# Performance work log

Measured on AMD Instinct MI355X. Metric: run time of the kernel, lower is better.

Reference implementation:

```python
import jax, jax.numpy as jnp
import numpy as np

B, N, E, H = 2, 2048, 1024, 16
D = E // H


def setup_inputs() -> dict:
    key = jax.random.key(0)
    ks = jax.random.split(key, 10)
    s = 0.02  # small init so softmax is well-conditioned
    return {
        "x": jax.random.normal(ks[0], (B, N, E), jnp.float32),
        "y": jax.random.normal(ks[1], (B, N, E), jnp.float32),
        # W stored as [in, out]; torch Linear computes x @ W_t.T + b, equivalent here.
        "Wq": jax.random.normal(ks[2], (E, E), jnp.float32) * s,
        "bq": jax.random.normal(ks[3], (E,), jnp.float32) * s,
        "Wk": jax.random.normal(ks[4], (E, E), jnp.float32) * s,
        "bk": jax.random.normal(ks[5], (E,), jnp.float32) * s,
        "Wv": jax.random.normal(ks[6], (E, E), jnp.float32) * s,
        "bv": jax.random.normal(ks[7], (E,), jnp.float32) * s,
        "Wo": jax.random.normal(ks[8], (E, E), jnp.float32) * s,
        "bo": jax.random.normal(ks[9], (E,), jnp.float32) * s,
    }


def _split_heads(t):
    # [b, n, (h d)] -> [b, h, n, d]
    b, n, e = t.shape
    return t.reshape(b, n, H, D).transpose(0, 2, 1, 3)


def reference(x, y, Wq, bq, Wk, bk, Wv, bv, Wo, bo):
    q = _split_heads(x @ Wq + bq)          # [b,h,n,d]
    k = _split_heads(y @ Wk + bk)
    v = _split_heads(y @ Wv + bv)
    energy = jnp.einsum('bhqd,bhkd->bhqk', q, k)            # [b,h,n,n]
    # Faithful quirk: softmax first, then divide by sqrt(emb_size).
    scaling = jnp.asarray(E, x.dtype) ** 0.5
    att = jax.nn.softmax(energy, axis=-1) / scaling
    out = jnp.einsum('bhqk,bhkd->bhqd', att, v)             # [b,h,n,d]
    out = out.transpose(0, 2, 1, 3).reshape(x.shape[0], x.shape[1], E)
    return out @ Wo + bo
```

## Files before the change

kernel.cpp:

```cpp
#include <hip/hip_runtime.h>
#include <stdint.h>

#define BATCH 2
#define SEQ   2048
#define EMB   1024
#define NH    16
#define HD    64
#define MROWS (BATCH*SEQ)
#define LOG2E 1.4426950408889634f

using bf16x8 = __attribute__((ext_vector_type(8))) short;
using f32x4  = __attribute__((ext_vector_type(4))) float;
using f32x16 = __attribute__((ext_vector_type(16))) float;

__device__ __forceinline__ unsigned short f2bf(float f) {
  __bf16 b = (__bf16)f;
  return __builtin_bit_cast(unsigned short, b);
}

__device__ __forceinline__ unsigned int cvtpk_bf16(float lo, float hi) {
  unsigned int w;
  asm("v_cvt_pk_bf16_f32 %0, %1, %2" : "=v"(w) : "v"(lo), "v"(hi));
  return w;
}

#if __has_builtin(__builtin_amdgcn_exp2f)
__device__ __forceinline__ float fast_exp2(float x) { return __builtin_amdgcn_exp2f(x); }
#else
__device__ __forceinline__ float fast_exp2(float x) {
  float r;
  asm("v_exp_f32 %0, %1\n\ts_nop 1" : "=v"(r) : "v"(x));
  return r;
}
#endif

__device__ __forceinline__ void async_load16(const void* g, void* l) {
  __builtin_amdgcn_global_load_lds(
      (__attribute__((address_space(1))) void*)g,
      (__attribute__((address_space(3))) void*)l,
      16, 0, 0);
}

__global__ __launch_bounds__(256) void convert_kernel(
    const float* __restrict__ in, unsigned short* __restrict__ out, int n4) {
  int i = blockIdx.x * blockDim.x + threadIdx.x;
  if (i >= n4) return;
  const float4 v = reinterpret_cast<const float4*>(in)[i];
  ushort4 o;
  o.x = f2bf(v.x); o.y = f2bf(v.y); o.z = f2bf(v.z); o.w = f2bf(v.w);
  reinterpret_cast<ushort4*>(out)[i] = o;
}

__global__ __launch_bounds__(256) void transw_kernel(
    const float* __restrict__ Wq, const float* __restrict__ Wk,
    const float* __restrict__ Wv, const float* __restrict__ Wo,
    unsigned short* __restrict__ WtAll) {
  const int z = blockIdx.z;
  const float* W = (z == 0) ? Wq : (z == 1) ? Wk : (z == 2) ? Wv : Wo;
  unsigned short* Wt = WtAll + (size_t)z * EMB * EMB;
  __shared__ unsigned short tile[64][65];
  const int tc = threadIdx.x & 15;
  const int tr = threadIdx.x >> 4;
  const int n0 = blockIdx.x * 64, k0 = blockIdx.y * 64;
#pragma unroll
  for (int rr = 0; rr < 4; ++rr) {
    const int row = rr * 16 + tr;
    float4 v = *reinterpret_cast<const float4*>(W + (size_t)(k0 + row) * EMB + n0 + tc * 4);
    tile[tc * 4 + 0][row] = f2bf(v.x);
    tile[tc * 4 + 1][row] = f2bf(v.y);
    tile[tc * 4 + 2][row] = f2bf(v.z);
    tile[tc * 4 + 3][row] = f2bf(v.w);
  }
  __syncthreads();
#pragma unroll
  for (int rr = 0; rr < 4; ++rr) {
    const int row = rr * 16 + tr;
    ushort4 o;
    o.x = tile[row][tc * 4 + 0];
    o.y = tile[row][tc * 4 + 1];
    o.z = tile[row][tc * 4 + 2];
    o.w = tile[row][tc * 4 + 3];
    *reinterpret_cast<ushort4*>(Wt + (size_t)(n0 + row) * EMB + k0 + tc * 4) = o;
  }
}

#define BM 128
#define BN 128
#define BK 32

__global__ __launch_bounds__(256, 2) void gemm_kernel(
    const unsigned short* __restrict__ xb,
    const unsigned short* __restrict__ yb,
    const unsigned short* __restrict__ attnb,
    const unsigned short* __restrict__ WtAll,
    const float* __restrict__ bq, const float* __restrict__ bk,
    const float* __restrict__ bv, const float* __restrict__ bo,
    unsigned short* __restrict__ Qb, unsigned short* __restrict__ Kb,
    unsigned short* __restrict__ Vt, float* __restrict__ dout,
    int phase) {
  __shared__ __align__(16) unsigned short As[BM * BK];
  __shared__ __align__(16) unsigned short Bs[BN * BK];

  const int z = blockIdx.z;
  const unsigned short* A;
  const unsigned short* Bt;
  const float* bias;
  int mode;
  if (phase == 0) {
    A    = (z == 0) ? xb : yb;
    Bt   = WtAll + (size_t)z * EMB * EMB;
    bias = (z == 0) ? bq : (z == 1) ? bk : bv;
    mode = z;
  } else {
    A = attnb; Bt = WtAll + (size_t)3 * EMB * EMB; bias = bo; mode = 3;
  }

  const int tid = threadIdx.x;
  const int lane = tid & 63, wid = tid >> 6;
  const int wr = wid >> 1, wc = wid & 1;
  const int l15 = lane & 15, l4 = lane >> 4;
  const int m0 = blockIdx.y * BM, n0 = blockIdx.x * BN;

  const int crow = tid >> 2;
  const int cslot = tid & 3;

  f32x4 acc[4][4] = {};

  for (int kt = 0; kt < EMB; kt += BK) {
#pragma unroll
    for (int it = 0; it < 2; ++it)
      async_load16(A + (size_t)(m0 + it * 64 + crow) * EMB + kt + cslot * 8,
                   (char*)As + it * 4096 + wid * 1024);
#pragma unroll
    for (int it = 0; it < 2; ++it)
      async_load16(Bt + (size_t)(n0 + it * 64 + crow) * EMB + kt + cslot * 8,
                   (char*)Bs + it * 4096 + wid * 1024);
    __syncthreads();

    bf16x8 af[4], bfr[4];
#pragma unroll
    for (int i = 0; i < 4; ++i) {
      af[i]  = *reinterpret_cast<const bf16x8*>((const char*)As + (wr * 64 + i * 16 + l15) * 64 + l4 * 16);
      bfr[i] = *reinterpret_cast<const bf16x8*>((const char*)Bs + (wc * 64 + i * 16 + l15) * 64 + l4 * 16);
    }
#pragma unroll
    for (int i = 0; i < 4; ++i)
#pragma unroll
      for (int j = 0; j < 4; ++j)
        acc[i][j] = __builtin_amdgcn_mfma_f32_16x16x32_bf16(af[i], bfr[j], acc[i][j], 0, 0, 0);
    __syncthreads();
  }

#pragma unroll
  for (int i = 0; i < 4; ++i) {
#pragma unroll
    for (int j = 0; j < 4; ++j) {
      const int col = n0 + wc * 64 + j * 16 + l15;
      const float bsv = bias[col];
#pragma unroll
      for (int r = 0; r < 4; ++r) {
        const int row = m0 + wr * 64 + i * 16 + l4 * 4 + r;
        const float v = acc[i][j][r] + bsv;
        if (mode == 3) {
          dout[(size_t)row * EMB + col] = v;
        } else {
          const int b = row >> 11, n = row & (SEQ - 1);
          const int h = col >> 6, d = col & (HD - 1);
          if (mode == 0)
            Qb[(((size_t)(b * NH + h)) * SEQ + n) * HD + d] = f2bf(v);
          else if (mode == 1)
            Kb[(((size_t)(b * NH + h)) * SEQ + n) * HD + d] = f2bf(v * LOG2E);
          else
            Vt[(((size_t)(b * NH + h)) * HD + d) * SEQ + n] = f2bf(v);
        }
      }
    }
  }
}

#define KVB 64
#define NT  (SEQ/KVB)

__global__ __launch_bounds__(256, 2) void flash_kernel(
    const unsigned short* __restrict__ Qb,
    const unsigned short* __restrict__ Kb,
    const unsigned short* __restrict__ Vt,
    unsigned short* __restrict__ attnb) {
  __shared__ __align__(16) char Ks[2][8192];
  __shared__ __align__(16) char Vs[2][8192];

  const int tid = threadIdx.x;
  const int lane = tid & 63, wid = tid >> 6;
  const int l31 = lane & 31, hi = lane >> 5;

  const int lin = blockIdx.x;
  const int swz = (lin & 7) * 64 + (lin >> 3);
  const int bh = swz >> 4;
  const int qt = swz & 15;
  const int bb = bh >> 4, hh = bh & 15;
  const int q0 = qt * 128 + wid * 32;

  const unsigned short* Qp = Qb + (size_t)bh * SEQ * HD;
  const unsigned short* Kp = Kb + (size_t)bh * SEQ * HD;
  const unsigned short* Vp = Vt + (size_t)bh * HD * SEQ;

  const int srow = tid >> 3;
  const int sslot = tid & 7;

  bf16x8 qf[4];
#pragma unroll
  for (int kt = 0; kt < 4; ++kt)
    qf[kt] = *reinterpret_cast<const bf16x8*>(Qp + (size_t)(q0 + l31) * HD + kt * 16 + hi * 8);

#define STAGE(b, kv)                                                        \
  {                                                                         \
    _Pragma("unroll")                                                       \
    for (int it = 0; it < 2; ++it) {                                        \
      const int r = it * 32 + srow;                                         \
      async_load16(Kp + (size_t)((kv) + r) * HD + ((sslot ^ (r & 7)) * 8),  \
                   Ks[b] + it * 4096 + tid * 16);                           \
      async_load16(Vp + (size_t)r * SEQ + (kv) + ((sslot ^ (r & 7)) * 8),   \
                   Vs[b] + it * 4096 + tid * 16);                           \
    }                                                                       \
  }

  STAGE(0, 0)
  STAGE(1, KVB)

  f32x16 accO[2] = {};
  float mI = -1e30f, lI = 0.f;

  for (int t = 0; t < NT; ++t) {
    const int buf = t & 1;
    if (t < NT - 1) {
      asm volatile("s_waitcnt vmcnt(4)" ::: "memory");
    } else {
      asm volatile("s_waitcnt vmcnt(0)" ::: "memory");
    }
    __builtin_amdgcn_s_barrier();
    __builtin_amdgcn_sched_barrier(0);

    bf16x8 kf[2][4];
#pragma unroll
    for (int t2 = 0; t2 < 2; ++t2)
#pragma unroll
      for (int kt = 0; kt < 4; ++kt) {
        const int key = t2 * 32 + l31;
        kf[t2][kt] = *reinterpret_cast<const bf16x8*>(
            Ks[buf] + key * 128 + (((kt * 2 + hi) ^ (key & 7)) * 16));
      }
    f32x16 sc[2] = {};
#pragma unroll
    for (int t2 = 0; t2 < 2; ++t2)
#pragma unroll
      for (int kt = 0; kt < 4; ++kt)
        sc[t2] = __builtin_amdgcn_mfma_f32_32x32x16_bf16(kf[t2][kt], qf[kt], sc[t2], 0, 0, 0);

    float mown = sc[0][0];
#pragma unroll
    for (int t2 = 0; t2 < 2; ++t2)
#pragma unroll
      for (int r = 0; r < 16; ++r) mown = fmaxf(mown, sc[t2][r]);
    mown = fmaxf(mown, __shfl_xor(mown, 32));

    if (!__all(mown - mI <= 8.0f)) {
      const float mnew = fmaxf(mI, mown);
      const float scl = fast_exp2(mI - mnew);
      mI = mnew;
      lI *= scl;
#pragma unroll
      for (int dt = 0; dt < 2; ++dt)
#pragma unroll
        for (int r = 0; r < 16; ++r) accO[dt][r] *= scl;
    }

    float p[2][16];
    float ls = 0.f;
#pragma unroll
    for (int t2 = 0; t2 < 2; ++t2)
#pragma unroll
      for (int r = 0; r < 16; ++r) {
        p[t2][r] = fast_exp2(sc[t2][r] - mI);
        ls += p[t2][r];
      }
    ls += __shfl_xor(ls, 32);
    lI += ls;

    bf16x8 pf[4];
#pragma unroll
    for (int kt = 0; kt < 4; ++kt) {
      const int t2 = kt >> 1, g = (kt & 1) * 8;
      const unsigned int Aw = cvtpk_bf16(p[t2][g + 0], p[t2][g + 1]);
      const unsigned int Cw = cvtpk_bf16(p[t2][g + 2], p[t2][g + 3]);
      const unsigned int Bw = cvtpk_bf16(p[t2][g + 4], p[t2][g + 5]);
      const unsigned int Dw = cvtpk_bf16(p[t2][g + 6], p[t2][g + 7]);
      const unsigned int s1 = hi ? Aw : Bw;
      const unsigned int r1 = __shfl_xor(s1, 32);
      const unsigned int s2 = hi ? Cw : Dw;
      const unsigned int r2 = __shfl_xor(s2, 32);
      union { unsigned int u[4]; bf16x8 v; } cvt;
      cvt.u[0] = hi ? r1 : Aw;
      cvt.u[1] = hi ? r2 : Cw;
      cvt.u[2] = hi ? Bw : r1;
      cvt.u[3] = hi ? Dw : r2;
      pf[kt] = cvt.v;
    }

    bf16x8 vf[2][4];
#pragma unroll
    for (int dt = 0; dt < 2; ++dt)
#pragma unroll
      for (int kt = 0; kt < 4; ++kt) {
        const int d = dt * 32 + l31;
        vf[dt][kt] = *reinterpret_cast<const bf16x8*>(
            Vs[buf] + d * 128 + (((kt * 2 + hi) ^ (d & 7)) * 16));
      }
#pragma unroll
    for (int dt = 0; dt < 2; ++dt)
#pragma unroll
      for (int kt = 0; kt < 4; ++kt)
        accO[dt] = __builtin_amdgcn_mfma_f32_32x32x16_bf16(vf[dt][kt], pf[kt], accO[dt], 0, 0, 0);

    __builtin_amdgcn_sched_barrier(0);
    __builtin_amdgcn_s_barrier();
    __builtin_amdgcn_sched_barrier(0);

    if (t + 2 < NT) {
      STAGE(buf, (t + 2) * KVB)
    }
  }

  const float inv = 1.0f / (lI * 32.0f);
  const size_t obase = ((size_t)(bb * SEQ + q0 + l31)) * EMB + hh * HD;
#pragma unroll
  for (int dt = 0; dt < 2; ++dt)
#pragma unroll
    for (int rr = 0; rr < 4; ++rr) {
      ushort4 o;
      o.x = f2bf(accO[dt][rr * 4 + 0] * inv);
      o.y = f2bf(accO[dt][rr * 4 + 1] * inv);
      o.z = f2bf(accO[dt][rr * 4 + 2] * inv);
      o.w = f2bf(accO[dt][rr * 4 + 3] * inv);
      *reinterpret_cast<ushort4*>(attnb + obase + dt * 32 + 8 * rr + 4 * hi) = o;
    }
}

extern "C" void kernel_launch(void* const* d_in, const int* in_sizes, int n_in,
                              void* d_out, int out_size, void* d_ws, size_t ws_size,
                              hipStream_t stream) {
  (void)in_sizes; (void)n_in; (void)out_size;
  const float* x  = (const float*)d_in[0];
  const float* y  = (const float*)d_in[1];
  const float* Wq = (const float*)d_in[2];
  const float* bq = (const float*)d_in[3];
  const float* Wk = (const float*)d_in[4];
  const float* bk = (const float*)d_in[5];
  const float* Wv = (const float*)d_in[6];
  const float* bv = (const float*)d_in[7];
  const float* Wo = (const float*)d_in[8];
  const float* bo = (const float*)d_in[9];
  float* out = (float*)d_out;

  char* ws = (char*)d_ws;
  unsigned short* xb    = (unsigned short*)(ws + (size_t)(0u  << 20));
  unsigned short* yb    = (unsigned short*)(ws + (size_t)(8u  << 20));
  unsigned short* WtAll = (unsigned short*)(ws + (size_t)(16u << 20));
  unsigned short* Qb    = (unsigned short*)(ws + (size_t)(24u << 20));
  unsigned short* Kb    = (unsigned short*)(ws + (size_t)(32u << 20));
  unsigned short* Vt    = (unsigned short*)(ws + (size_t)(40u << 20));
  unsigned short* attnb = (unsigned short*)(ws + (size_t)(48u << 20));
  if (ws_size < ((size_t)56u << 20)) return;

  const int n4 = (BATCH * SEQ * EMB) / 4;
  hipLaunchKernelGGL(convert_kernel, dim3(n4 / 256), dim3(256), 0, stream, x, xb, n4);
  hipLaunchKernelGGL(convert_kernel, dim3(n4 / 256), dim3(256), 0, stream, y, yb, n4);
  hipLaunchKernelGGL(transw_kernel, dim3(16, 16, 4), dim3(256), 0, stream, Wq, Wk, Wv, Wo, WtAll);
  hipLaunchKernelGGL(gemm_kernel, dim3(EMB / BN, MROWS / BM, 3), dim3(256), 0, stream,
                     xb, yb, attnb, WtAll, bq, bk, bv, bo, Qb, Kb, Vt, out, 0);
  hipLaunchKernelGGL(flash_kernel, dim3(SEQ / 128 * BATCH * NH), dim3(256), 0, stream,
                     Qb, Kb, Vt, attnb);
  hipLaunchKernelGGL(gemm_kernel, dim3(EMB / BN, MROWS / BM, 1), dim3(256), 0, stream,
                     xb, yb, attnb, WtAll, bq, bk, bv, bo, Qb, Kb, Vt, out, 1);
}
```

Baseline: 145.6 us.

## Triple-buffer GEMM and flash-attention LDS stages; use permlane32 swap for cross-half exchange

Both the projection GEMM and the flash-attention loop now use a three-slot LDS ring. The load for step s+2 is issued right after the single barrier at the top of each iteration, so the second barrier per iteration goes away and global-to-LDS copies overlap compute. The flash kernel also replaces ds_bpermute-based __shfl_xor(…,32) exchanges for the max, the sum and the P fragment repacking with the permlane32_swap builtin when it is available. The cost is 50% more LDS per block, which may reduce occupancy, and the GEMM now waits with vmcnt counting.

```diff
diff --git a/kernel.cpp b/kernel.cpp
--- a/kernel.cpp
+++ b/kernel.cpp
@@ -33,6 +33,32 @@
   return r;
 }
 #endif
+
+__device__ __forceinline__ void swap32(unsigned int& a, unsigned int& b, int hi) {
+#if __has_builtin(__builtin_amdgcn_permlane32_swap)
+  (void)hi;
+  typedef unsigned int u32x2_t __attribute__((ext_vector_type(2)));
+  u32x2_t r = __builtin_amdgcn_permlane32_swap(a, b, false, false);
+  a = r[0]; b = r[1];
+#else
+  const unsigned int ca = __shfl_xor(a, 32), cb = __shfl_xor(b, 32);
+  const unsigned int na = hi ? cb : a;
+  const unsigned int nb = hi ? b : ca;
+  a = na; b = nb;
+#endif
+}
+
+__device__ __forceinline__ float xmax32(float x, int hi) {
+  unsigned int a = __builtin_bit_cast(unsigned int, x), b = a;
+  swap32(a, b, hi);
+  return fmaxf(__builtin_bit_cast(float, a), __builtin_bit_cast(float, b));
+}
+
+__device__ __forceinline__ float xadd32(float x, int hi) {
+  unsigned int a = __builtin_bit_cast(unsigned int, x), b = a;
+  swap32(a, b, hi);
+  return __builtin_bit_cast(float, a) + __builtin_bit_cast(float, b);
+}
 
 __device__ __forceinline__ void async_load16(const void* g, void* l) {
   __builtin_amdgcn_global_load_lds(
@@ -87,6 +113,7 @@
 #define BM 128
 #define BN 128
 #define BK 32
+#define NKS (EMB/BK)
 
 __global__ __launch_bounds__(256, 2) void gemm_kernel(
     const unsigned short* __restrict__ xb,
@@ -98,8 +125,8 @@
     unsigned short* __restrict__ Qb, unsigned short* __restrict__ Kb,
     unsigned short* __restrict__ Vt, float* __restrict__ dout,
     int phase) {
-  __shared__ __align__(16) unsigned short As[BM * BK];
-  __shared__ __align__(16) unsigned short Bs[BN * BK];
+  __shared__ __align__(16) unsigned short As[3][BM * BK];
+  __shared__ __align__(16) unsigned short Bs[3][BN * BK];
 
   const int z = blockIdx.z;
   const unsigned short* A;
@@ -124,32 +151,52 @@
   const int crow = tid >> 2;
   const int cslot = tid & 3;
 
+#define GSTAGE(b, kt)                                                          \
+  {                                                                            \
+    _Pragma("unroll")                                                          \
+    for (int it = 0; it < 2; ++it)                                             \
+      async_load16(A + (size_t)(m0 + it * 64 + crow) * EMB + (kt) + cslot * 8, \
+                   (char*)As[b] + it * 4096 + wid * 1024);                     \
+    _Pragma("unroll")                                                          \
+    for (int it = 0; it < 2; ++it)                                             \
+      async_load16(Bt + (size_t)(n0 + it * 64 + crow) * EMB + (kt) + cslot * 8,\
+                   (char*)Bs[b] + it * 4096 + wid * 1024);                     \
+  }
+
+  GSTAGE(0, 0)
+  GSTAGE(1, BK)
+
   f32x4 acc[4][4] = {};
 
-  for (int kt = 0; kt < EMB; kt += BK) {
-#pragma unroll
-    for (int it = 0; it < 2; ++it)
-      async_load16(A + (size_t)(m0 + it * 64 + crow) * EMB + kt + cslot * 8,
-                   (char*)As + it * 4096 + wid * 1024);
-#pragma unroll
-    for (int it = 0; it < 2; ++it)
-      async_load16(Bt + (size_t)(n0 + it * 64 + crow) * EMB + kt + cslot * 8,
-                   (char*)Bs + it * 4096 + wid * 1024);
-    __syncthreads();
+  int buf = 0, sb = 2;
+  for (int s = 0; s < NKS; ++s) {
+    __builtin_amdgcn_sched_barrier(0);
+    if (s < NKS - 1) {
+      asm volatile("s_waitcnt vmcnt(4)" ::: "memory");
+    } else {
+      asm volatile("s_waitcnt vmcnt(0)" ::: "memory");
+    }
+    __builtin_amdgcn_s_barrier();
+    __builtin_amdgcn_sched_barrier(0);
+
+    if (s + 2 < NKS) { GSTAGE(sb, (s + 2) * BK) }
 
     bf16x8 af[4], bfr[4];
 #pragma unroll
     for (int i = 0; i < 4; ++i) {
-      af[i]  = *reinterpret_cast<const bf16x8*>((const char*)As + (wr * 64 + i * 16 + l15) * 64 + l4 * 16);
-      bfr[i] = *reinterpret_cast<const bf16x8*>((const char*)Bs + (wc * 64 + i * 16 + l15) * 64 + l4 * 16);
+      af[i]  = *reinterpret_cast<const bf16x8*>((const char*)As[buf] + (wr * 64 + i * 16 + l15) * 64 + l4 * 16);
+      bfr[i] = *reinterpret_cast<const bf16x8*>((const char*)Bs[buf] + (wc * 64 + i * 16 + l15) * 64 + l4 * 16);
     }
 #pragma unroll
     for (int i = 0; i < 4; ++i)
 #pragma unroll
       for (int j = 0; j < 4; ++j)
         acc[i][j] = __builtin_amdgcn_mfma_f32_16x16x32_bf16(af[i], bfr[j], acc[i][j], 0, 0, 0);
-    __syncthreads();
-  }
+
+    buf = (buf == 2) ? 0 : buf + 1;
+    sb  = (sb  == 2) ? 0 : sb + 1;
+  }
+#undef GSTAGE
 
 #pragma unroll
   for (int i = 0; i < 4; ++i) {
@@ -186,8 +233,8 @@
     const unsigned short* __restrict__ Kb,
     const unsigned short* __restrict__ Vt,
     unsigned short* __restrict__ attnb) {
-  __shared__ __align__(16) char Ks[2][8192];
-  __shared__ __align__(16) char Vs[2][8192];
+  __shared__ __align__(16) char Ks[3][8192];
+  __shared__ __align__(16) char Vs[3][8192];
 
   const int tid = threadIdx.x;
   const int lane = tid & 63, wid = tid >> 6;
@@ -230,8 +277,9 @@
   f32x16 accO[2] = {};
   float mI = -1e30f, lI = 0.f;
 
+  int buf = 0, sb = 2;
   for (int t = 0; t < NT; ++t) {
-    const int buf = t & 1;
+    __builtin_amdgcn_sched_barrier(0);
     if (t < NT - 1) {
       asm volatile("s_waitcnt vmcnt(4)" ::: "memory");
     } else {
@@ -239,6 +287,8 @@
     }
     __builtin_amdgcn_s_barrier();
     __builtin_amdgcn_sched_barrier(0);
+
+    if (t + 2 < NT) { STAGE(sb, (t + 2) * KVB) }
 
     bf16x8 kf[2][4];
 #pragma unroll
@@ -261,7 +311,7 @@
     for (int t2 = 0; t2 < 2; ++t2)
 #pragma unroll
       for (int r = 0; r < 16; ++r) mown = fmaxf(mown, sc[t2][r]);
-    mown = fmaxf(mown, __shfl_xor(mown, 32));
+    mown = xmax32(mown, hi);
 
     if (!__all(mown - mI <= 8.0f)) {
       const float mnew = fmaxf(mI, mown);
@@ -283,26 +333,20 @@
         p[t2][r] = fast_exp2(sc[t2][r] - mI);
         ls += p[t2][r];
       }
-    ls += __shfl_xor(ls, 32);
-    lI += ls;
+    lI += xadd32(ls, hi);
 
     bf16x8 pf[4];
 #pragma unroll
     for (int kt = 0; kt < 4; ++kt) {
       const int t2 = kt >> 1, g = (kt & 1) * 8;
-      const unsigned int Aw = cvtpk_bf16(p[t2][g + 0], p[t2][g + 1]);
-      const unsigned int Cw = cvtpk_bf16(p[t2][g + 2], p[t2][g + 3]);
-      const unsigned int Bw = cvtpk_bf16(p[t2][g + 4], p[t2][g + 5]);
-      const unsigned int Dw = cvtpk_bf16(p[t2][g + 6], p[t2][g + 7]);
-      const unsigned int s1 = hi ? Aw : Bw;
-      const unsigned int r1 = __shfl_xor(s1, 32);
-      const unsigned int s2 = hi ? Cw : Dw;
-      const unsigned int r2 = __shfl_xor(s2, 32);
+      unsigned int Aw = cvtpk_bf16(p[t2][g + 0], p[t2][g + 1]);
+      unsigned int Cw = cvtpk_bf16(p[t2][g + 2], p[t2][g + 3]);
+      unsigned int Bw = cvtpk_bf16(p[t2][g + 4], p[t2][g + 5]);
+      unsigned int Dw = cvtpk_bf16(p[t2][g + 6], p[t2][g + 7]);
+      swap32(Aw, Bw, hi);
+      swap32(Cw, Dw, hi);
       union { unsigned int u[4]; bf16x8 v; } cvt;
-      cvt.u[0] = hi ? r1 : Aw;
-      cvt.u[1] = hi ? r2 : Cw;
-      cvt.u[2] = hi ? Bw : r1;
-      cvt.u[3] = hi ? Dw : r2;
+      cvt.u[0] = Aw; cvt.u[1] = Cw; cvt.u[2] = Bw; cvt.u[3] = Dw;
       pf[kt] = cvt.v;
     }
 
@@ -321,14 +365,10 @@
       for (int kt = 0; kt < 4; ++kt)
         accO[dt] = __builtin_amdgcn_mfma_f32_32x32x16_bf16(vf[dt][kt], pf[kt], accO[dt], 0, 0, 0);
 
-    __builtin_amdgcn_sched_barrier(0);
-    __builtin_amdgcn_s_barrier();
-    __builtin_amdgcn_sched_barrier(0);
-
-    if (t + 2 < NT) {
-      STAGE(buf, (t + 2) * KVB)
-    }
-  }
+    buf = (buf == 2) ? 0 : buf + 1;
+    sb  = (sb  == 2) ? 0 : sb + 1;
+  }
+#undef STAGE
 
   const float inv = 1.0f / (lI * 32.0f);
   const size_t obase = ((size_t)(bb * SEQ + q0 + l31)) * EMB + hh * HD;
```

Result: faster. 138.6 us (-4.9%).
